# Kernel optimization log

Hardware: AMD Instinct MI355X
Metric: run time of the kernel (lower is better)

Reference implementation:

```python
import jax, jax.numpy as jnp
import numpy as np

FEATURE_DIM = 128
N_NODES = 100000
N_EDGES = 800000
L1_IN = 2 * FEATURE_DIM            # 256
L1_OUT = int((2 * FEATURE_DIM) ** 0.5)  # 16
L2_DIM = L1_OUT + 1                # 17


def leaky(x):
    return jnp.where(x >= 0, x, 0.1 * x)


def setup_inputs() -> dict:
    key = jax.random.key(0)
    ks = jax.random.split(key, 8)
    Jt_ind = jax.random.randint(ks[0], (2, N_EDGES), 0, N_NODES)
    Jt_val = jax.random.normal(ks[1], (N_EDGES,), dtype=jnp.float32)
    f = jax.random.normal(ks[2], (N_NODES, FEATURE_DIM), dtype=jnp.float32)
    W1 = jax.random.normal(ks[3], (L1_IN, L1_OUT), dtype=jnp.float32) * (1.0 / np.sqrt(L1_IN))
    b1 = jnp.zeros((L1_OUT,), dtype=jnp.float32)
    W2 = jax.random.normal(ks[4], (L2_DIM, L2_DIM), dtype=jnp.float32) * (1.0 / np.sqrt(L2_DIM))
    b2 = jnp.zeros((L2_DIM,), dtype=jnp.float32)
    Wc = jax.random.normal(ks[5], (L2_DIM, 1), dtype=jnp.float32) * (1.0 / np.sqrt(L2_DIM))
    bc = jnp.ones((1,), dtype=jnp.float32)  # collapse_bias = 1
    return {"Jt_ind": Jt_ind, "Jt_val": Jt_val, "f": f, "N": N_NODES,
            "W1": W1, "b1": b1, "W2": W2, "b2": b2, "Wc": Wc, "bc": bc}


def reference(Jt_ind, Jt_val, f, N, W1, b1, W2, b2, Wc, bc):
    i = Jt_ind[0]
    j = Jt_ind[1]
    absv = jnp.abs(Jt_val)                                     # [E]
    # degree: per-destination sum of |Jt_val|
    deg_abs = jax.ops.segment_sum(absv, i, num_segments=N)     # [N]
    Jt_val_abs_norm = absv / deg_abs[i]                        # [E]
    # gather endpoint features and run tiny edge-MLP
    x = jnp.concatenate([f[i], f[j]], axis=1)                  # [E, 2F]
    x = leaky(x @ W1 + b1)                                     # [E, L1_OUT]
    x = jnp.concatenate([x, Jt_val_abs_norm[:, None]], axis=1) # [E, L2_DIM]
    x = leaky(x @ W2 + b2)                                     # [E, L2_DIM]
    e_values = (x @ Wc + bc)[:, 0]                             # [E]
    # segment softmax over edges grouped by destination i (stable)
    m = jax.ops.segment_max(e_values, i, num_segments=N)       # [N]
    ex = jnp.exp(e_values - m[i])                              # [E]
    s = jax.ops.segment_sum(ex, i, num_segments=N)             # [N]
    return ex / s[i]                                           # [E]
```

## Files before the change

kernel.cpp:

```cpp
#include <hip/hip_runtime.h>
#include <hip/hip_fp16.h>
#include <math.h>

#define FDIM  128
#define L1OUT 16
#define L2DIM 17
#define TR    64
#define TSTR  129

struct __align__(16) H16 { __half2 h[8]; };

__device__ __forceinline__ float lrelu(float v) { return v >= 0.f ? v : 0.1f * v; }

__global__ void node_transform(const float* __restrict__ f,
                               const float* __restrict__ W1,
                               H16* __restrict__ A, H16* __restrict__ B,
                               float* __restrict__ deg, float* __restrict__ ssum,
                               int N) {
    __shared__ float tile[TR * TSTR];
    __shared__ float w1s[256 * L1OUT];

    int t   = threadIdx.x;
    int gid = blockIdx.x * 256 + t;
    if (gid < N) { deg[gid] = 0.f; ssum[gid] = 0.f; }

    {
        const float4* src = reinterpret_cast<const float4*>(W1);
        float4*       dst = reinterpret_cast<float4*>(w1s);
#pragma unroll
        for (int q = 0; q < 4; ++q) dst[t + 256 * q] = src[t + 256 * q];
    }
    int base = blockIdx.x * TR;
#pragma unroll
    for (int q = 0; q < 8; ++q) {
        int i4 = t + 256 * q;
        int r  = i4 >> 5;
        int c4 = i4 & 31;
        float4 v = make_float4(0.f, 0.f, 0.f, 0.f);
        if (base + r < N)
            v = reinterpret_cast<const float4*>(f + (size_t)(base + r) * FDIM)[c4];
        float* d = &tile[r * TSTR + c4 * 4];
        d[0] = v.x; d[1] = v.y; d[2] = v.z; d[3] = v.w;
    }
    __syncthreads();

    int lane    = t & 63;
    int w       = t >> 6;
    int colbase = (w & 1) * 8;
    int krowoff = (w >> 1) * FDIM;

    float acc[8];
#pragma unroll
    for (int c = 0; c < 8; ++c) acc[c] = 0.f;

    const float* trow  = &tile[lane * TSTR];
    const float* wbase = &w1s[krowoff * L1OUT + colbase];
#pragma unroll 4
    for (int k = 0; k < FDIM; ++k) {
        float x = trow[k];
        const float4* wr = reinterpret_cast<const float4*>(wbase + k * L1OUT);
        float4 w0 = wr[0], w1v = wr[1];
        acc[0] += x * w0.x;  acc[1] += x * w0.y;
        acc[2] += x * w0.z;  acc[3] += x * w0.w;
        acc[4] += x * w1v.x; acc[5] += x * w1v.y;
        acc[6] += x * w1v.z; acc[7] += x * w1v.w;
    }

    int n = base + lane;
    if (n < N) {
        __half2 h[4];
#pragma unroll
        for (int q = 0; q < 4; ++q)
            h[q] = __floats2half2_rn(acc[2 * q], acc[2 * q + 1]);
        H16* arr = (w >> 1) ? B : A;
        float4* dst = reinterpret_cast<float4*>(
            reinterpret_cast<char*>(arr + n) + (w & 1) * 16);
        *dst = *reinterpret_cast<float4*>(h);
    }
}

__global__ void deg_accum(const int* __restrict__ ind_i, const float* __restrict__ val,
                          float* __restrict__ deg, int E) {
    int t = blockIdx.x * blockDim.x + threadIdx.x;
    int e = t * 4;
    if (e + 3 < E) {
        int4   ii = *reinterpret_cast<const int4*>(ind_i + e);
        float4 vv = *reinterpret_cast<const float4*>(val + e);
        atomicAdd(&deg[ii.x], fabsf(vv.x));
        atomicAdd(&deg[ii.y], fabsf(vv.y));
        atomicAdd(&deg[ii.z], fabsf(vv.z));
        atomicAdd(&deg[ii.w], fabsf(vv.w));
    } else {
        for (; e < E; ++e) atomicAdd(&deg[ind_i[e]], fabsf(val[e]));
    }
}

__global__ void edge_mlp(const int* __restrict__ ind, const float* __restrict__ val,
                         const H16* __restrict__ A, const H16* __restrict__ B,
                         const float* __restrict__ deg,
                         const float* __restrict__ b1,
                         const float* __restrict__ W2, const float* __restrict__ b2,
                         const float* __restrict__ Wc, const float* __restrict__ bc,
                         float* __restrict__ eout, float* __restrict__ ssum, int E) {
    __shared__ float w2s[L2DIM * 20];
    __shared__ float b1s[L1OUT];
    __shared__ float b2s[L2DIM];
    __shared__ float wcs[L2DIM];
    __shared__ float bc0s;

    int t = threadIdx.x;
    for (int idx = t; idx < L2DIM * L2DIM; idx += 256) {
        int c = idx / L2DIM, r = idx % L2DIM;
        w2s[c * 20 + r] = W2[idx];
    }
    if (t < L1OUT) b1s[t] = b1[t];
    if (t < L2DIM) b2s[t] = b2[t];
    if (t < L2DIM) wcs[t] = Wc[t];
    if (t == 0)    bc0s   = bc[0];
    __syncthreads();

    int e = blockIdx.x * 256 + t;
    if (e >= E) return;

    int i = ind[e];
    int j = ind[E + e];
    H16 a  = A[i];
    H16 bb = B[j];
    float v  = val[e];
    float dg = deg[i];

    float x[L2DIM];
#pragma unroll
    for (int q = 0; q < 8; ++q) {
        float2 fa = __half22float2(a.h[q]);
        float2 fb = __half22float2(bb.h[q]);
        x[2 * q]     = lrelu(fa.x + fb.x + b1s[2 * q]);
        x[2 * q + 1] = lrelu(fa.y + fb.y + b1s[2 * q + 1]);
    }
    x[L1OUT] = fabsf(v) / dg;

    float acc[L2DIM];
#pragma unroll
    for (int r = 0; r < L2DIM; ++r) acc[r] = b2s[r];
#pragma unroll
    for (int c = 0; c < L2DIM; ++c) {
        float xc = x[c];
        const float4* r4 = reinterpret_cast<const float4*>(&w2s[c * 20]);
        float4 w0 = r4[0], w1 = r4[1], w2v = r4[2], w3 = r4[3];
        float  w16 = w2s[c * 20 + 16];
        acc[0]  += xc * w0.x;  acc[1]  += xc * w0.y;
        acc[2]  += xc * w0.z;  acc[3]  += xc * w0.w;
        acc[4]  += xc * w1.x;  acc[5]  += xc * w1.y;
        acc[6]  += xc * w1.z;  acc[7]  += xc * w1.w;
        acc[8]  += xc * w2v.x; acc[9]  += xc * w2v.y;
        acc[10] += xc * w2v.z; acc[11] += xc * w2v.w;
        acc[12] += xc * w3.x;  acc[13] += xc * w3.y;
        acc[14] += xc * w3.z;  acc[15] += xc * w3.w;
        acc[16] += xc * w16;
    }
    float ev = bc0s;
#pragma unroll
    for (int r = 0; r < L2DIM; ++r) ev += lrelu(acc[r]) * wcs[r];

    float ex = __expf(ev);
    eout[e] = ex;
    atomicAdd(&ssum[i], ex);
}

__global__ void normalize(const int* __restrict__ ind_i, const float* __restrict__ ssum,
                          float* __restrict__ ex, int E) {
    int t = blockIdx.x * blockDim.x + threadIdx.x;
    int e = t * 4;
    if (e + 3 < E) {
        int4   ii = *reinterpret_cast<const int4*>(ind_i + e);
        float4 vv = *reinterpret_cast<const float4*>(ex + e);
        vv.x /= ssum[ii.x];
        vv.y /= ssum[ii.y];
        vv.z /= ssum[ii.z];
        vv.w /= ssum[ii.w];
        *reinterpret_cast<float4*>(ex + e) = vv;
    } else {
        for (; e < E; ++e) ex[e] = ex[e] / ssum[ind_i[e]];
    }
}

extern "C" void kernel_launch(void* const* d_in, const int* in_sizes, int n_in,
                              void* d_out, int out_size, void* d_ws, size_t ws_size,
                              hipStream_t stream) {
    const int*   Jt_ind = (const int*)  d_in[0];
    const float* Jt_val = (const float*)d_in[1];
    const float* f      = (const float*)d_in[2];
    const float* W1 = (const float*)d_in[4];
    const float* b1 = (const float*)d_in[5];
    const float* W2 = (const float*)d_in[6];
    const float* b2 = (const float*)d_in[7];
    const float* Wc = (const float*)d_in[8];
    const float* bc = (const float*)d_in[9];

    const int E = in_sizes[1];
    const int N = in_sizes[2] / FDIM;
    float* out = (float*)d_out;

    char* ws = (char*)d_ws;
    H16*   A    = (H16*)ws;    ws += (size_t)N * sizeof(H16);
    H16*   Bm   = (H16*)ws;    ws += (size_t)N * sizeof(H16);
    float* deg  = (float*)ws;  ws += (size_t)N * sizeof(float);
    float* ssum = (float*)ws;  ws += (size_t)N * sizeof(float);

    const int B256 = 256;
    const int nblk = (N + TR - 1) / TR;
    const int eblk = (E + B256 - 1) / B256;
    const int qblk = ((E + 3) / 4 + B256 - 1) / B256;

    node_transform<<<nblk, B256, 0, stream>>>(f, W1, A, Bm, deg, ssum, N);
    deg_accum     <<<qblk, B256, 0, stream>>>(Jt_ind, Jt_val, deg, E);
    edge_mlp      <<<eblk, B256, 0, stream>>>(Jt_ind, Jt_val, A, Bm, deg,
                                              b1, W2, b2, Wc, bc, out, ssum, E);
    normalize     <<<qblk, B256, 0, stream>>>(Jt_ind, ssum, out, E);
}
```

Measured before the change: 232.9 us.

## Fuse degree accumulation into node transform, fold b1, two edges per thread

The degree atomic accumulation is merged into the node_transform kernel as a grid-stride loop, which removes one launch. The deg/ssum zeroing moves to a hipMemsetAsync. The b1 bias is folded into the A projection so edge_mlp no longer adds it. W1 is read from global or cache instead of being staged in LDS, the tile stride is changed to allow float4 LDS stores and loads, and edge_mlp handles two edges per thread with vectorized index, value and output accesses. Together these aim to cut launch overhead and improve memory-level parallelism, at the cost of higher register pressure and W1 loads that bypass LDS.

```diff
diff --git a/kernel.cpp b/kernel.cpp
--- a/kernel.cpp
+++ b/kernel.cpp
@@ -6,31 +6,43 @@
 #define L1OUT 16
 #define L2DIM 17
 #define TR    64
-#define TSTR  129
+#define TSTR  132
 
 struct __align__(16) H16 { __half2 h[8]; };
 
 __device__ __forceinline__ float lrelu(float v) { return v >= 0.f ? v : 0.1f * v; }
 
-__global__ void node_transform(const float* __restrict__ f,
-                               const float* __restrict__ W1,
-                               H16* __restrict__ A, H16* __restrict__ B,
-                               float* __restrict__ deg, float* __restrict__ ssum,
-                               int N) {
-    __shared__ float tile[TR * TSTR];
-    __shared__ float w1s[256 * L1OUT];
-
-    int t   = threadIdx.x;
-    int gid = blockIdx.x * 256 + t;
-    if (gid < N) { deg[gid] = 0.f; ssum[gid] = 0.f; }
+__global__ __launch_bounds__(256, 4) void node_transform(
+    const float* __restrict__ f, const float* __restrict__ W1,
+    const float* __restrict__ b1,
+    const int* __restrict__ ind_i, const float* __restrict__ val,
+    H16* __restrict__ A, H16* __restrict__ B,
+    float* __restrict__ deg, int N, int E)
+{
+    __shared__ __align__(16) float tile[TR * TSTR];
+
+    const int t    = threadIdx.x;
+    const int gtid = blockIdx.x * 256 + t;
+    const int GT   = gridDim.x * 256;
 
     {
-        const float4* src = reinterpret_cast<const float4*>(W1);
-        float4*       dst = reinterpret_cast<float4*>(w1s);
-#pragma unroll
-        for (int q = 0; q < 4; ++q) dst[t + 256 * q] = src[t + 256 * q];
-    }
-    int base = blockIdx.x * TR;
+        const int E4 = E >> 2;
+        for (int q = gtid; q < E4; q += GT) {
+            int e = q << 2;
+            int4   ii = *reinterpret_cast<const int4*>(ind_i + e);
+            float4 vv = *reinterpret_cast<const float4*>(val + e);
+            atomicAdd(&deg[ii.x], fabsf(vv.x));
+            atomicAdd(&deg[ii.y], fabsf(vv.y));
+            atomicAdd(&deg[ii.z], fabsf(vv.z));
+            atomicAdd(&deg[ii.w], fabsf(vv.w));
+        }
+        if (gtid < (E & 3)) {
+            int e = (E & ~3) + gtid;
+            atomicAdd(&deg[ind_i[e]], fabsf(val[e]));
+        }
+    }
+
+    const int base = blockIdx.x * TR;
 #pragma unroll
     for (int q = 0; q < 8; ++q) {
         int i4 = t + 256 * q;
@@ -39,132 +51,137 @@
         float4 v = make_float4(0.f, 0.f, 0.f, 0.f);
         if (base + r < N)
             v = reinterpret_cast<const float4*>(f + (size_t)(base + r) * FDIM)[c4];
-        float* d = &tile[r * TSTR + c4 * 4];
-        d[0] = v.x; d[1] = v.y; d[2] = v.z; d[3] = v.w;
+        *reinterpret_cast<float4*>(&tile[r * TSTR + c4 * 4]) = v;
     }
     __syncthreads();
 
-    int lane    = t & 63;
-    int w       = t >> 6;
-    int colbase = (w & 1) * 8;
-    int krowoff = (w >> 1) * FDIM;
+    const int lane    = t & 63;
+    const int w       = t >> 6;
+    const int colbase = (w & 1) * 8;
+    const int isB     = w >> 1;
+    const float* wbase = W1 + (size_t)(isB * FDIM) * L1OUT + colbase;
 
     float acc[8];
 #pragma unroll
-    for (int c = 0; c < 8; ++c) acc[c] = 0.f;
-
-    const float* trow  = &tile[lane * TSTR];
-    const float* wbase = &w1s[krowoff * L1OUT + colbase];
-#pragma unroll 4
-    for (int k = 0; k < FDIM; ++k) {
-        float x = trow[k];
-        const float4* wr = reinterpret_cast<const float4*>(wbase + k * L1OUT);
-        float4 w0 = wr[0], w1v = wr[1];
-        acc[0] += x * w0.x;  acc[1] += x * w0.y;
-        acc[2] += x * w0.z;  acc[3] += x * w0.w;
-        acc[4] += x * w1v.x; acc[5] += x * w1v.y;
-        acc[6] += x * w1v.z; acc[7] += x * w1v.w;
+    for (int c = 0; c < 8; ++c) acc[c] = isB ? 0.f : b1[colbase + c];
+
+    const float* trow = &tile[lane * TSTR];
+#pragma unroll 2
+    for (int k4 = 0; k4 < FDIM / 4; ++k4) {
+        float4 xv = *reinterpret_cast<const float4*>(trow + k4 * 4);
+#pragma unroll
+        for (int u = 0; u < 4; ++u) {
+            float x = (u == 0) ? xv.x : (u == 1) ? xv.y : (u == 2) ? xv.z : xv.w;
+            const float* wr = wbase + (size_t)(k4 * 4 + u) * L1OUT;
+            float4 w0  = *reinterpret_cast<const float4*>(wr);
+            float4 w1v = *reinterpret_cast<const float4*>(wr + 4);
+            acc[0] += x * w0.x;  acc[1] += x * w0.y;
+            acc[2] += x * w0.z;  acc[3] += x * w0.w;
+            acc[4] += x * w1v.x; acc[5] += x * w1v.y;
+            acc[6] += x * w1v.z; acc[7] += x * w1v.w;
+        }
     }
 
     int n = base + lane;
     if (n < N) {
-        __half2 h[4];
+        __align__(16) __half2 h[4];
 #pragma unroll
         for (int q = 0; q < 4; ++q)
             h[q] = __floats2half2_rn(acc[2 * q], acc[2 * q + 1]);
-        H16* arr = (w >> 1) ? B : A;
+        H16* arr = isB ? B : A;
         float4* dst = reinterpret_cast<float4*>(
             reinterpret_cast<char*>(arr + n) + (w & 1) * 16);
         *dst = *reinterpret_cast<float4*>(h);
     }
 }
 
-__global__ void deg_accum(const int* __restrict__ ind_i, const float* __restrict__ val,
-                          float* __restrict__ deg, int E) {
-    int t = blockIdx.x * blockDim.x + threadIdx.x;
-    int e = t * 4;
-    if (e + 3 < E) {
-        int4   ii = *reinterpret_cast<const int4*>(ind_i + e);
-        float4 vv = *reinterpret_cast<const float4*>(val + e);
-        atomicAdd(&deg[ii.x], fabsf(vv.x));
-        atomicAdd(&deg[ii.y], fabsf(vv.y));
-        atomicAdd(&deg[ii.z], fabsf(vv.z));
-        atomicAdd(&deg[ii.w], fabsf(vv.w));
-    } else {
-        for (; e < E; ++e) atomicAdd(&deg[ind_i[e]], fabsf(val[e]));
-    }
-}
-
-__global__ void edge_mlp(const int* __restrict__ ind, const float* __restrict__ val,
-                         const H16* __restrict__ A, const H16* __restrict__ B,
-                         const float* __restrict__ deg,
-                         const float* __restrict__ b1,
-                         const float* __restrict__ W2, const float* __restrict__ b2,
-                         const float* __restrict__ Wc, const float* __restrict__ bc,
-                         float* __restrict__ eout, float* __restrict__ ssum, int E) {
+__global__ __launch_bounds__(256, 4) void edge_mlp(
+    const int* __restrict__ ind, const float* __restrict__ val,
+    const H16* __restrict__ A, const H16* __restrict__ B,
+    const float* __restrict__ deg,
+    const float* __restrict__ W2, const float* __restrict__ b2,
+    const float* __restrict__ Wc, const float* __restrict__ bc,
+    float* __restrict__ eout, float* __restrict__ ssum, int E)
+{
     __shared__ float w2s[L2DIM * 20];
-    __shared__ float b1s[L1OUT];
     __shared__ float b2s[L2DIM];
     __shared__ float wcs[L2DIM];
     __shared__ float bc0s;
 
-    int t = threadIdx.x;
+    const int t = threadIdx.x;
     for (int idx = t; idx < L2DIM * L2DIM; idx += 256) {
-        int c = idx / L2DIM, r = idx % L2DIM;
+        int c = idx / L2DIM, r = idx - c * L2DIM;
         w2s[c * 20 + r] = W2[idx];
     }
-    if (t < L1OUT) b1s[t] = b1[t];
     if (t < L2DIM) b2s[t] = b2[t];
     if (t < L2DIM) wcs[t] = Wc[t];
     if (t == 0)    bc0s   = bc[0];
     __syncthreads();
 
-    int e = blockIdx.x * 256 + t;
-    if (e >= E) return;
-
-    int i = ind[e];
-    int j = ind[E + e];
-    H16 a  = A[i];
-    H16 bb = B[j];
-    float v  = val[e];
-    float dg = deg[i];
-
-    float x[L2DIM];
-#pragma unroll
-    for (int q = 0; q < 8; ++q) {
-        float2 fa = __half22float2(a.h[q]);
-        float2 fb = __half22float2(bb.h[q]);
-        x[2 * q]     = lrelu(fa.x + fb.x + b1s[2 * q]);
-        x[2 * q + 1] = lrelu(fa.y + fb.y + b1s[2 * q + 1]);
-    }
-    x[L1OUT] = fabsf(v) / dg;
-
-    float acc[L2DIM];
-#pragma unroll
-    for (int r = 0; r < L2DIM; ++r) acc[r] = b2s[r];
-#pragma unroll
-    for (int c = 0; c < L2DIM; ++c) {
-        float xc = x[c];
-        const float4* r4 = reinterpret_cast<const float4*>(&w2s[c * 20]);
-        float4 w0 = r4[0], w1 = r4[1], w2v = r4[2], w3 = r4[3];
-        float  w16 = w2s[c * 20 + 16];
-        acc[0]  += xc * w0.x;  acc[1]  += xc * w0.y;
-        acc[2]  += xc * w0.z;  acc[3]  += xc * w0.w;
-        acc[4]  += xc * w1.x;  acc[5]  += xc * w1.y;
-        acc[6]  += xc * w1.z;  acc[7]  += xc * w1.w;
-        acc[8]  += xc * w2v.x; acc[9]  += xc * w2v.y;
-        acc[10] += xc * w2v.z; acc[11] += xc * w2v.w;
-        acc[12] += xc * w3.x;  acc[13] += xc * w3.y;
-        acc[14] += xc * w3.z;  acc[15] += xc * w3.w;
-        acc[16] += xc * w16;
-    }
-    float ev = bc0s;
-#pragma unroll
-    for (int r = 0; r < L2DIM; ++r) ev += lrelu(acc[r]) * wcs[r];
-
-    float ex = __expf(ev);
-    eout[e] = ex;
-    atomicAdd(&ssum[i], ex);
+    const int e0 = (blockIdx.x * 256 + t) * 2;
+    if (e0 >= E) return;
+    const bool has1 = (e0 + 1) < E;
+
+    int2 ii = *reinterpret_cast<const int2*>(ind + e0);
+    int  j0 = ind[E + e0];
+    int  j1 = has1 ? ind[E + e0 + 1] : j0;
+    float2 vv = *reinterpret_cast<const float2*>(val + e0);
+    int i0 = ii.x, i1 = has1 ? ii.y : ii.x;
+
+    H16 a0 = A[i0], bb0 = B[j0];
+    H16 a1 = A[i1], bb1 = B[j1];
+    float dg0 = deg[i0];
+    float dg1 = deg[i1];
+
+    float ex[2];
+#pragma unroll
+    for (int s = 0; s < 2; ++s) {
+        const H16& a  = s ? a1 : a0;
+        const H16& bb = s ? bb1 : bb0;
+        float nv = fabsf(s ? vv.y : vv.x) / (s ? dg1 : dg0);
+
+        float x[L2DIM];
+#pragma unroll
+        for (int q = 0; q < 8; ++q) {
+            float2 fa = __half22float2(a.h[q]);
+            float2 fb = __half22float2(bb.h[q]);
+            x[2 * q]     = lrelu(fa.x + fb.x);
+            x[2 * q + 1] = lrelu(fa.y + fb.y);
+        }
+        x[L1OUT] = nv;
+
+        float acc[L2DIM];
+#pragma unroll
+        for (int r = 0; r < L2DIM; ++r) acc[r] = b2s[r];
+#pragma unroll
+        for (int c = 0; c < L2DIM; ++c) {
+            float xc = x[c];
+            const float4* r4 = reinterpret_cast<const float4*>(&w2s[c * 20]);
+            float4 w0 = r4[0], w1v = r4[1], w2v = r4[2], w3 = r4[3];
+            float  w16 = w2s[c * 20 + 16];
+            acc[0]  += xc * w0.x;  acc[1]  += xc * w0.y;
+            acc[2]  += xc * w0.z;  acc[3]  += xc * w0.w;
+            acc[4]  += xc * w1v.x; acc[5]  += xc * w1v.y;
+            acc[6]  += xc * w1v.z; acc[7]  += xc * w1v.w;
+            acc[8]  += xc * w2v.x; acc[9]  += xc * w2v.y;
+            acc[10] += xc * w2v.z; acc[11] += xc * w2v.w;
+            acc[12] += xc * w3.x;  acc[13] += xc * w3.y;
+            acc[14] += xc * w3.z;  acc[15] += xc * w3.w;
+            acc[16] += xc * w16;
+        }
+        float ev = bc0s;
+#pragma unroll
+        for (int r = 0; r < L2DIM; ++r) ev += lrelu(acc[r]) * wcs[r];
+        ex[s] = __expf(ev);
+    }
+
+    atomicAdd(&ssum[i0], ex[0]);
+    if (has1) {
+        atomicAdd(&ssum[i1], ex[1]);
+        *reinterpret_cast<float2*>(eout + e0) = make_float2(ex[0], ex[1]);
+    } else {
+        eout[e0] = ex[0];
+    }
 }
 
 __global__ void normalize(const int* __restrict__ ind_i, const float* __restrict__ ssum,
@@ -202,19 +219,20 @@
     float* out = (float*)d_out;
 
     char* ws = (char*)d_ws;
+    float* deg  = (float*)ws;  ws += (size_t)N * sizeof(float);
+    float* ssum = (float*)ws;  ws += (size_t)N * sizeof(float);
     H16*   A    = (H16*)ws;    ws += (size_t)N * sizeof(H16);
     H16*   Bm   = (H16*)ws;    ws += (size_t)N * sizeof(H16);
-    float* deg  = (float*)ws;  ws += (size_t)N * sizeof(float);
-    float* ssum = (float*)ws;  ws += (size_t)N * sizeof(float);
 
     const int B256 = 256;
     const int nblk = (N + TR - 1) / TR;
-    const int eblk = (E + B256 - 1) / B256;
+    const int eblk = ((E + 1) / 2 + B256 - 1) / B256;
     const int qblk = ((E + 3) / 4 + B256 - 1) / B256;
 
-    node_transform<<<nblk, B256, 0, stream>>>(f, W1, A, Bm, deg, ssum, N);
-    deg_accum     <<<qblk, B256, 0, stream>>>(Jt_ind, Jt_val, deg, E);
+    hipMemsetAsync(deg, 0, 2 * (size_t)N * sizeof(float), stream);
+    node_transform<<<nblk, B256, 0, stream>>>(f, W1, b1, Jt_ind, Jt_val,
+                                              A, Bm, deg, N, E);
     edge_mlp      <<<eblk, B256, 0, stream>>>(Jt_ind, Jt_val, A, Bm, deg,
-                                              b1, W2, b2, Wc, bc, out, ssum, E);
+                                              W2, b2, Wc, bc, out, ssum, E);
     normalize     <<<qblk, B256, 0, stream>>>(Jt_ind, ssum, out, E);
 }
```

After: 561.9 us. 2.41x slower.
